# Kernel optimization log

Hardware: AMD Instinct MI355X
Metric: run time of the kernel (lower is better)

Reference implementation:

```python
import jax, jax.numpy as jnp
import numpy as np

B, T, D, H = 2, 2048, 1024, 16
HD = D // H  # head_dim = 64


def setup_inputs() -> dict:
    key = jax.random.key(0)
    ks = jax.random.split(key, 6)
    x = jax.random.normal(ks[0], (B, T, D), dtype=jnp.float32)
    wq = jax.random.normal(ks[1], (D, D), dtype=jnp.float32) * (D ** -0.5)
    wk = jax.random.normal(ks[2], (D, D), dtype=jnp.float32) * (D ** -0.5)
    wv = jax.random.normal(ks[3], (D, D), dtype=jnp.float32) * (D ** -0.5)
    wo = jax.random.normal(ks[4], (D, D), dtype=jnp.float32) * (D ** -0.5)
    # RoPE tables: standard inverse-frequency angles, shape [T, head_dim]
    inv_freq = 1.0 / (10000.0 ** (jnp.arange(0, HD, 2, dtype=jnp.float32) / HD))
    ang = jnp.arange(T, dtype=jnp.float32)[:, None] * inv_freq[None, :]  # [T, HD/2]
    ang = jnp.concatenate([ang, ang], axis=-1)  # [T, HD]
    cos, sin = jnp.cos(ang), jnp.sin(ang)
    # causal mask [1,1,T,T]: True where attention is allowed
    mask = jnp.tril(jnp.ones((T, T), dtype=bool))[None, None]
    return {"x": x, "wq": wq, "wk": wk, "wv": wv, "wo": wo,
            "cos": cos, "sin": sin, "mask": mask}


def rotate_half(u):
    u1, u2 = jnp.split(u, 2, axis=-1)
    return jnp.concatenate([-u2, u1], axis=-1)


def reference(x, wq, wk, wv, wo, cos, sin, mask):
    b, t, c = x.shape
    # projections (nn.Linear: y = x @ W^T), reshape to [B, H, T, HD]
    def proj(w):
        return (x @ w.T).reshape(b, t, H, HD).transpose(0, 2, 1, 3)
    q, k, v = proj(wq), proj(wk), proj(wv)
    # inline RoPE: cos/sin broadcast [1,1,T,HD]
    co = cos[:t][None, None]
    si = sin[:t][None, None]
    q = q * co + rotate_half(q) * si
    k = k * co + rotate_half(k) * si
    # scaled dot-product attention with causal mask
    att = jnp.einsum("bhqd,bhkd->bhqk", q, k) * (HD ** -0.5)
    att = jnp.where(mask[:, :, :t, :t], att, -jnp.inf)
    att = jax.nn.softmax(att, axis=-1)
    out = jnp.einsum("bhqk,bhkd->bhqd", att, v)
    out = out.transpose(0, 2, 1, 3).reshape(b, t, c)
    return out @ wo.T
```

## Files before the change

### kernel.cpp

```cpp
#include <hip/hip_runtime.h>
#include <hip/hip_bf16.h>
#include <type_traits>

#define B_  2
#define T_  2048
#define D_  1024
#define H_  16
#define HD_ 64

typedef __attribute__((ext_vector_type(8))) short bf16x8;
typedef __attribute__((ext_vector_type(4))) float f32x4;

__device__ __forceinline__ unsigned short f2b(float x) {
  union { __hip_bfloat16 h; unsigned short u; } c;
  c.h = __float2bfloat16(x);
  return c.u;
}

__device__ __forceinline__ void ld_g2l_16(const unsigned short* g, unsigned short* l) {
  auto gp = (const __attribute__((address_space(1))) unsigned int*)g;
  auto lp = (__attribute__((address_space(3))) unsigned int*)l;
  __builtin_amdgcn_global_load_lds(gp, lp, 16, 0, 0);
}

__device__ __forceinline__ void cast_job(int blk, const float* __restrict__ x,
                                         const float* __restrict__ wq, const float* __restrict__ wk,
                                         const float* __restrict__ wv, const float* __restrict__ wo,
                                         unsigned short* __restrict__ xb,
                                         unsigned short* __restrict__ wp) {
  const float* src;
  unsigned short* dst;
  size_t off;
  if (blk < 2048) {
    src = x; dst = xb; off = (size_t)blk * 2048;
  } else {
    int t = (blk - 2048) >> 9;
    int r = (blk - 2048) & 511;
    src = (t == 0) ? wq : (t == 1) ? wk : (t == 2) ? wv : wo;
    dst = wp + (size_t)t * 1048576;
    off = (size_t)r * 2048;
  }
  size_t i = off + threadIdx.x * 8;
  float4 a = *(const float4*)(src + i);
  float4 b = *(const float4*)(src + i + 4);
  unsigned short h[8] = {f2b(a.x), f2b(a.y), f2b(a.z), f2b(a.w),
                         f2b(b.x), f2b(b.y), f2b(b.z), f2b(b.w)};
  *(uint4*)(dst + i) = *(uint4*)h;
}

template <typename OutT, int MROWS>
__device__ __forceinline__ void gemm_core(unsigned short* __restrict__ shm,
                                          const unsigned short* __restrict__ A,
                                          const unsigned short* __restrict__ Bw,
                                          OutT* __restrict__ C, int K, int Ldc,
                                          int rope_mode, const float* __restrict__ cosT,
                                          const float* __restrict__ sinT, int tok0) {
  constexpr int MT = MROWS / 32;
  constexpr int ASZ = MROWS * 32;
  const int tid = threadIdx.x;
  const int lane = tid & 63;
  const int w = tid >> 6;
  const int m16 = lane & 15;
  const int quad = lane >> 4;
  const int wm = w >> 1, wn = w & 1;
  const int rl = lane >> 2;
  const int cl = (lane & 3) * 8;

  f32x4 acc[MT][4];
#pragma unroll
  for (int i = 0; i < MT; i++)
#pragma unroll
    for (int j = 0; j < 4; j++) acc[i][j] = (f32x4){0.f, 0.f, 0.f, 0.f};

  auto stage = [&](int it, int bs) {
    int k0 = it * 32;
#pragma unroll
    for (int t = 0; t < MROWS / 64; t++) {
      int seg = w * 16 + t * 64;
      ld_g2l_16(A + (size_t)(seg + rl) * K + k0 + cl, shm + bs * ASZ + seg * 32);
    }
#pragma unroll
    for (int j2 = 0; j2 < 2; j2++) {
      int seg = w * 32 + j2 * 16;
      ld_g2l_16(Bw + (size_t)(seg + rl) * K + k0 + cl, shm + 2 * ASZ + bs * 4096 + seg * 32);
    }
  };

  const int nit = K / 32;
  stage(0, 0);
  __syncthreads();
  for (int it = 0; it < nit; it++) {
    int cur = it & 1;
    if (it + 1 < nit) stage(it + 1, cur ^ 1);
    bf16x8 af[MT], bfr[4];
#pragma unroll
    for (int mt = 0; mt < MT; mt++)
      af[mt] = *(const bf16x8*)(shm + cur * ASZ + (wm * (MT * 16) + mt * 16 + m16) * 32 + quad * 8);
#pragma unroll
    for (int nt = 0; nt < 4; nt++)
      bfr[nt] = *(const bf16x8*)(shm + 2 * ASZ + cur * 4096 + (wn * 64 + nt * 16 + m16) * 32 + quad * 8);
#pragma unroll
    for (int mt = 0; mt < MT; mt++)
#pragma unroll
      for (int nt = 0; nt < 4; nt++)
        acc[mt][nt] = __builtin_amdgcn_mfma_f32_16x16x32_bf16(af[mt], bfr[nt], acc[mt][nt], 0, 0, 0);
    __syncthreads();
  }

  if (rope_mode == 3) {
    if constexpr (std::is_same_v<OutT, unsigned short> && MROWS == 64) {
#pragma unroll
      for (int mt = 0; mt < MT; mt++)
#pragma unroll
        for (int nt = 0; nt < 4; nt++) {
          int lc = wn * 64 + nt * 16 + m16;
          int s  = wm * 8 + mt * 4 + quad;
          int ph = s ^ (lc & 15);
          unsigned short pk[4] = {f2b(acc[mt][nt][0]), f2b(acc[mt][nt][1]),
                                  f2b(acc[mt][nt][2]), f2b(acc[mt][nt][3])};
          *(uint2*)&shm[lc * 64 + ph * 4] = *(uint2*)pk;
        }
      __syncthreads();
#pragma unroll
      for (int i = 0; i < 8; i++) {
        int li = i * 256 + tid;
        int r = li >> 4, c2 = li & 15;
        int ph = c2 ^ (r & 15);
        *(uint2*)(C + (size_t)r * T_ + c2 * 4) = *(const uint2*)&shm[r * 64 + ph * 4];
      }
    }
    return;
  }

  if (rope_mode == 1 || rope_mode == 2) {
    float scale = (rope_mode == 2) ? 0.18033688011112042f : 1.f;
#pragma unroll
    for (int mt = 0; mt < MT; mt++)
#pragma unroll
      for (int reg = 0; reg < 4; reg++) {
        int t = (tok0 + wm * (MT * 16) + mt * 16 + quad * 4 + reg) & (T_ - 1);
#pragma unroll
        for (int nt = 0; nt < 2; nt++) {
          int d = nt * 16 + m16;
          float co = cosT[t * HD_ + d] * scale;
          float si = sinT[t * HD_ + d] * scale;
          float lo = acc[mt][nt][reg], hi = acc[mt][nt + 2][reg];
          acc[mt][nt][reg]     = lo * co - hi * si;
          acc[mt][nt + 2][reg] = hi * co + lo * si;
        }
      }
  }
#pragma unroll
  for (int mt = 0; mt < MT; mt++)
#pragma unroll
    for (int nt = 0; nt < 4; nt++)
#pragma unroll
      for (int reg = 0; reg < 4; reg++) {
        OutT* p = C + (size_t)(wm * (MT * 16) + mt * 16 + quad * 4 + reg) * Ldc + wn * 64 + nt * 16 + m16;
        if constexpr (std::is_same_v<OutT, float>) *p = acc[mt][nt][reg];
        else *p = f2b(acc[mt][nt][reg]);
      }
}

__device__ __forceinline__ void qkv_job(unsigned short* shm, int nb, int bm,
                                        const unsigned short* __restrict__ xb,
                                        const unsigned short* __restrict__ wp,
                                        unsigned short* __restrict__ qkv,
                                        const float* __restrict__ cosT,
                                        const float* __restrict__ sinT) {
  const int mi = nb >> 3;
  const int bn = (nb & 7) * 128;
  if (mi == 2) {
    unsigned short* Cv = qkv + 2 * (4096ull * D_) +
                         (size_t)(bm >> 11) * (size_t)(H_ * HD_) * T_ +
                         (size_t)bn * T_ + (bm & (T_ - 1));
    gemm_core<unsigned short, 64>(shm, xb + (size_t)bm * D_,
                                  wp + (size_t)(2 * 1024 + bn) * D_,
                                  Cv, D_, T_, 3, nullptr, nullptr, bm);
  } else {
    const int rope_mode = (mi == 0) ? 2 : 1;
    gemm_core<unsigned short, 64>(shm, xb + (size_t)bm * D_,
                                  wp + (size_t)(mi * 1024 + bn) * D_,
                                  qkv + (size_t)mi * (4096ull * D_) + (size_t)bm * D_ + bn,
                                  D_, D_, rope_mode, cosT, sinT, bm);
  }
}

__device__ __forceinline__ void attn_job(unsigned short* pool, int x,
                                         const unsigned short* __restrict__ Q,
                                         const unsigned short* __restrict__ K,
                                         const unsigned short* __restrict__ VT,
                                         unsigned short* __restrict__ O) {
  unsigned short* qp = pool;
  unsigned short* ks = pool + 4096;
  unsigned short* vs = pool + 4096 + 8192;

  const int tid = threadIdx.x;
  const int lane = tid & 63;
  const int w = tid >> 6;
  const int m16 = lane & 15;
  const int quad = lane >> 4;
  const int swz = m16 & 7;
  const int pc0 = quad ^ swz;
  const int pc1 = pc0 ^ 4;

  const int qt = 31 - (x >> 5);
  const int bh = x & 31;
  const int b = bh >> 4, h = bh & 15;
  const int q0 = qt * 64;

  const unsigned short* Qb = Q + ((size_t)b * T_ + q0) * D_ + h * HD_;
  const unsigned short* Kb = K + (size_t)b * T_ * D_ + h * HD_;
  const unsigned short* VTb = VT + ((size_t)b * H_ + h) * HD_ * T_;

#pragma unroll
  for (int i = 0; i < 2; i++) {
    int idx = tid + i * 256;
    int r = idx >> 3, c = idx & 7;
    *(bf16x8*)&qp[r * 64 + ((c ^ (r & 7)) * 8)] = *(const bf16x8*)(Qb + (size_t)r * D_ + c * 8);
  }

  auto stage_kv = [&](int kt, int bs) {
    int rs = lane >> 3;
    int cs = ((lane & 7) ^ rs) * 8;
    int gr = w * 16 + rs;
    ld_g2l_16(Kb + (size_t)(kt * 64 + gr) * D_ + cs,      ks + bs * 4096 + (w * 16) * 64);
    ld_g2l_16(Kb + (size_t)(kt * 64 + gr + 8) * D_ + cs,  ks + bs * 4096 + (w * 16 + 8) * 64);
    ld_g2l_16(VTb + (size_t)gr * T_ + kt * 64 + cs,       vs + bs * 4096 + (w * 16) * 64);
    ld_g2l_16(VTb + (size_t)(gr + 8) * T_ + kt * 64 + cs, vs + bs * 4096 + (w * 16 + 8) * 64);
  };

  f32x4 o_acc[4];
#pragma unroll
  for (int dt = 0; dt < 4; dt++) o_acc[dt] = (f32x4){0.f, 0.f, 0.f, 0.f};
  float m_i = -1e30f, l_i = 0.f;
  const int row = w * 16 + m16;
  const int rs7 = row & 7;
  const int rg = q0 + row;

  const short one_bf = (short)0x3F80;
  bf16x8 ones = {one_bf, one_bf, one_bf, one_bf, one_bf, one_bf, one_bf, one_bf};

  stage_kv(0, 0);
  __syncthreads();
  bf16x8 q_frag[2];
  q_frag[0] = *(const bf16x8*)&qp[row * 64 + ((quad ^ rs7) * 8)];
  q_frag[1] = *(const bf16x8*)&qp[row * 64 + (((4 + quad) ^ rs7) * 8)];

  for (int t = 0; t <= qt; t++) {
    int cur = t & 1;
    if (t < qt) stage_kv(t + 1, cur ^ 1);

    const unsigned short* kc = ks + cur * 4096;
    const unsigned short* vc = vs + cur * 4096;
    f32x4 sf[4];
    __builtin_amdgcn_s_setprio(1);
#pragma unroll
    for (int jt = 0; jt < 4; jt++) {
      bf16x8 a0 = *(const bf16x8*)&kc[(jt * 16 + m16) * 64 + pc0 * 8];
      bf16x8 a1 = *(const bf16x8*)&kc[(jt * 16 + m16) * 64 + pc1 * 8];
      f32x4 acc = (f32x4){0.f, 0.f, 0.f, 0.f};
      acc = __builtin_amdgcn_mfma_f32_16x16x32_bf16(a0, q_frag[0], acc, 0, 0, 0);
      acc = __builtin_amdgcn_mfma_f32_16x16x32_bf16(a1, q_frag[1], acc, 0, 0, 0);
      sf[jt] = acc;
    }
    __builtin_amdgcn_s_setprio(0);
    if (t == qt) {
#pragma unroll
      for (int jt = 0; jt < 4; jt++)
#pragma unroll
        for (int reg = 0; reg < 4; reg++) {
          int jg = t * 64 + jt * 16 + quad * 4 + reg;
          if (jg > rg) sf[jt][reg] = -1e30f;
        }
    }
    float mx = sf[0][0];
#pragma unroll
    for (int jt = 0; jt < 4; jt++)
#pragma unroll
      for (int reg = 0; reg < 4; reg++) mx = fmaxf(mx, sf[jt][reg]);
    mx = fmaxf(mx, __shfl_xor(mx, 16, 64));
    mx = fmaxf(mx, __shfl_xor(mx, 32, 64));
    if (!__all(mx <= m_i + 8.f)) {
      float mn = fmaxf(m_i, mx);
      float alpha = exp2f(m_i - mn);
      l_i *= alpha;
#pragma unroll
      for (int dt = 0; dt < 4; dt++)
#pragma unroll
        for (int reg = 0; reg < 4; reg++) o_acc[dt][reg] *= alpha;
      m_i = mn;
    }
    float p[4][4];
#pragma unroll
    for (int jt = 0; jt < 4; jt++)
#pragma unroll
      for (int reg = 0; reg < 4; reg++)
        p[jt][reg] = exp2f(sf[jt][reg] - m_i);
#pragma unroll
    for (int jt = 0; jt < 4; jt++) {
      unsigned short pk[4] = {f2b(p[jt][0]), f2b(p[jt][1]), f2b(p[jt][2]), f2b(p[jt][3])};
      int cL = jt * 2 + (quad >> 1);
      *(uint2*)&qp[row * 64 + ((cL ^ rs7) * 8) + (quad & 1) * 4] = *(uint2*)pk;
    }
    bf16x8 bp0 = *(const bf16x8*)&qp[row * 64 + ((quad ^ rs7) * 8)];
    bf16x8 bp1 = *(const bf16x8*)&qp[row * 64 + (((4 + quad) ^ rs7) * 8)];
    f32x4 lacc = (f32x4){0.f, 0.f, 0.f, 0.f};
    lacc = __builtin_amdgcn_mfma_f32_16x16x32_bf16(ones, bp0, lacc, 0, 0, 0);
    lacc = __builtin_amdgcn_mfma_f32_16x16x32_bf16(ones, bp1, lacc, 0, 0, 0);
    __builtin_amdgcn_s_setprio(1);
#pragma unroll
    for (int dt = 0; dt < 4; dt++) {
      int rowd = dt * 16 + m16;
      bf16x8 a0 = *(const bf16x8*)&vc[rowd * 64 + pc0 * 8];
      bf16x8 a1 = *(const bf16x8*)&vc[rowd * 64 + pc1 * 8];
      o_acc[dt] = __builtin_amdgcn_mfma_f32_16x16x32_bf16(a0, bp0, o_acc[dt], 0, 0, 0);
      o_acc[dt] = __builtin_amdgcn_mfma_f32_16x16x32_bf16(a1, bp1, o_acc[dt], 0, 0, 0);
    }
    __builtin_amdgcn_s_setprio(0);
    l_i += lacc[0];
    __syncthreads();
  }

  float inv = 1.f / l_i;
#pragma unroll
  for (int dt = 0; dt < 4; dt++) {
    unsigned short ok[4];
#pragma unroll
    for (int reg = 0; reg < 4; reg++) ok[reg] = f2b(o_acc[dt][reg] * inv);
    int cL = dt * 2 + (quad >> 1);
    *(uint2*)&qp[row * 64 + ((cL ^ rs7) * 8) + (quad & 1) * 4] = *(uint2*)ok;
  }
  __syncthreads();
  unsigned short* Ob = O + ((size_t)b * T_ + q0) * D_ + h * HD_;
#pragma unroll
  for (int i = 0; i < 2; i++) {
    int idx = tid + i * 256;
    int r = idx >> 3, c = idx & 7;
    *(bf16x8*)(Ob + (size_t)r * D_ + c * 8) = *(const bf16x8*)&qp[r * 64 + ((c ^ (r & 7)) * 8)];
  }
}

__global__ void __launch_bounds__(256)
cast_all(const float* __restrict__ x, const float* __restrict__ wq,
         const float* __restrict__ wk, const float* __restrict__ wv,
         const float* __restrict__ wo, unsigned short* __restrict__ xb,
         unsigned short* __restrict__ wp) {
  cast_job(blockIdx.x, x, wq, wk, wv, wo, xb, wp);
}

__global__ void __launch_bounds__(256, 6)
gemm_qkv(const unsigned short* __restrict__ xb, const unsigned short* __restrict__ wp,
         unsigned short* __restrict__ qkv, const float* __restrict__ cosT,
         const float* __restrict__ sinT) {
  __shared__ __align__(16) unsigned short shm[12288];
  qkv_job(shm, blockIdx.x, blockIdx.y * 64, xb, wp, qkv, cosT, sinT);
}

__global__ void __launch_bounds__(256)
gemm_out(const unsigned short* __restrict__ Ab, const unsigned short* __restrict__ wob,
         float* __restrict__ C) {
  __shared__ __align__(16) unsigned short shm[12288];
  const int bn = blockIdx.x * 128;
  const int bm = blockIdx.y * 64;
  gemm_core<float, 64>(shm, Ab + (size_t)bm * D_, wob + (size_t)bn * D_,
                       C + (size_t)bm * D_ + bn, D_, D_, 0, nullptr, nullptr, 0);
}

__global__ void __launch_bounds__(256, 4)
attn_kernel(const unsigned short* __restrict__ Q, const unsigned short* __restrict__ K,
            const unsigned short* __restrict__ VT, unsigned short* __restrict__ O) {
  __shared__ __align__(16) unsigned short pool[20480];
  attn_job(pool, blockIdx.x, Q, K, VT, O);
}

extern "C" void kernel_launch(void* const* d_in, const int* in_sizes, int n_in,
                              void* d_out, int out_size, void* d_ws, size_t ws_size,
                              hipStream_t stream) {
  const float* x    = (const float*)d_in[0];
  const float* wq   = (const float*)d_in[1];
  const float* wk   = (const float*)d_in[2];
  const float* wv   = (const float*)d_in[3];
  const float* wo   = (const float*)d_in[4];
  const float* cosT = (const float*)d_in[5];
  const float* sinT = (const float*)d_in[6];
  float* out = (float*)d_out;

  const size_t NTOK = (size_t)B_ * T_;
  const size_t SZ   = NTOK * D_;
  unsigned short* xb   = (unsigned short*)d_ws;
  unsigned short* Wp   = xb + SZ;
  unsigned short* QKVh = Wp + 4 * 1048576;
  unsigned short* Ab   = QKVh + 3 * SZ;

  cast_all<<<4096, 256, 0, stream>>>(x, wq, wk, wv, wo, xb, Wp);
  gemm_qkv<<<dim3(24, 64), 256, 0, stream>>>(xb, Wp, QKVh, cosT, sinT);
  attn_kernel<<<1024, 256, 0, stream>>>(QKVh, QKVh + SZ, QKVh + 2 * SZ, Ab);
  gemm_out<<<dim3(8, 64), 256, 0, stream>>>(Ab, Wp + 3 * 1048576, out);
}
```

Baseline: 204.5 us.

## Double GEMM K-tile to 64 with XOR-swizzled LDS layout

The shared GEMM core now stages 64-wide K slices instead of 32, halving the number of main-loop iterations and barriers, and issues two MFMAs per fragment pair per iteration. The LDS layout switches to 64-element rows with an XOR swizzle on 16-byte chunks, meant to avoid bank conflicts on the fragment reads. The QKV and output GEMM kernels double their shared buffers to fit the larger tiles, and their occupancy hint drops to 3 blocks, which lowers the number of resident waves available to hide latency.

```diff
diff --git a/kernel.cpp b/kernel.cpp
--- a/kernel.cpp
+++ b/kernel.cpp
@@ -56,15 +56,19 @@
                                           int rope_mode, const float* __restrict__ cosT,
                                           const float* __restrict__ sinT, int tok0) {
   constexpr int MT = MROWS / 32;
-  constexpr int ASZ = MROWS * 32;
+  constexpr int ASZ = MROWS * 64;
+  constexpr int BSZ = 128 * 64;
   const int tid = threadIdx.x;
   const int lane = tid & 63;
   const int w = tid >> 6;
   const int m16 = lane & 15;
   const int quad = lane >> 4;
   const int wm = w >> 1, wn = w & 1;
-  const int rl = lane >> 2;
-  const int cl = (lane & 3) * 8;
+  const int rs = lane >> 3;
+  const int cs8 = ((lane & 7) ^ rs) * 8;
+  const int swz = m16 & 7;
+  const int pc0 = quad ^ swz;
+  const int pc1 = pc0 ^ 4;
 
   f32x4 acc[MT][4];
 #pragma unroll
@@ -73,37 +77,46 @@
     for (int j = 0; j < 4; j++) acc[i][j] = (f32x4){0.f, 0.f, 0.f, 0.f};
 
   auto stage = [&](int it, int bs) {
-    int k0 = it * 32;
-#pragma unroll
-    for (int t = 0; t < MROWS / 64; t++) {
-      int seg = w * 16 + t * 64;
-      ld_g2l_16(A + (size_t)(seg + rl) * K + k0 + cl, shm + bs * ASZ + seg * 32);
-    }
-#pragma unroll
-    for (int j2 = 0; j2 < 2; j2++) {
-      int seg = w * 32 + j2 * 16;
-      ld_g2l_16(Bw + (size_t)(seg + rl) * K + k0 + cl, shm + 2 * ASZ + bs * 4096 + seg * 32);
+    int k0 = it * 64;
+#pragma unroll
+    for (int t = 0; t < MROWS / 32; t++) {
+      int r0 = w * (MROWS / 4) + t * 8;
+      ld_g2l_16(A + (size_t)(r0 + rs) * K + k0 + cs8, shm + bs * ASZ + r0 * 64);
+    }
+#pragma unroll
+    for (int j = 0; j < 4; j++) {
+      int r0 = w * 32 + j * 8;
+      ld_g2l_16(Bw + (size_t)(r0 + rs) * K + k0 + cs8,
+                shm + 2 * ASZ + bs * BSZ + r0 * 64);
     }
   };
 
-  const int nit = K / 32;
+  const int nit = K / 64;
   stage(0, 0);
   __syncthreads();
   for (int it = 0; it < nit; it++) {
     int cur = it & 1;
     if (it + 1 < nit) stage(it + 1, cur ^ 1);
-    bf16x8 af[MT], bfr[4];
+    bf16x8 af[MT][2], bfr[4][2];
+#pragma unroll
+    for (int mt = 0; mt < MT; mt++) {
+      const unsigned short* ab = shm + cur * ASZ + (wm * (MT * 16) + mt * 16 + m16) * 64;
+      af[mt][0] = *(const bf16x8*)(ab + pc0 * 8);
+      af[mt][1] = *(const bf16x8*)(ab + pc1 * 8);
+    }
+#pragma unroll
+    for (int nt = 0; nt < 4; nt++) {
+      const unsigned short* bb = shm + 2 * ASZ + cur * BSZ + (wn * 64 + nt * 16 + m16) * 64;
+      bfr[nt][0] = *(const bf16x8*)(bb + pc0 * 8);
+      bfr[nt][1] = *(const bf16x8*)(bb + pc1 * 8);
+    }
 #pragma unroll
     for (int mt = 0; mt < MT; mt++)
-      af[mt] = *(const bf16x8*)(shm + cur * ASZ + (wm * (MT * 16) + mt * 16 + m16) * 32 + quad * 8);
-#pragma unroll
-    for (int nt = 0; nt < 4; nt++)
-      bfr[nt] = *(const bf16x8*)(shm + 2 * ASZ + cur * 4096 + (wn * 64 + nt * 16 + m16) * 32 + quad * 8);
-#pragma unroll
-    for (int mt = 0; mt < MT; mt++)
-#pragma unroll
-      for (int nt = 0; nt < 4; nt++)
-        acc[mt][nt] = __builtin_amdgcn_mfma_f32_16x16x32_bf16(af[mt], bfr[nt], acc[mt][nt], 0, 0, 0);
+#pragma unroll
+      for (int nt = 0; nt < 4; nt++) {
+        acc[mt][nt] = __builtin_amdgcn_mfma_f32_16x16x32_bf16(af[mt][0], bfr[nt][0], acc[mt][nt], 0, 0, 0);
+        acc[mt][nt] = __builtin_amdgcn_mfma_f32_16x16x32_bf16(af[mt][1], bfr[nt][1], acc[mt][nt], 0, 0, 0);
+      }
     __syncthreads();
   }
 
@@ -221,9 +234,9 @@
   }
 
   auto stage_kv = [&](int kt, int bs) {
-    int rs = lane >> 3;
-    int cs = ((lane & 7) ^ rs) * 8;
-    int gr = w * 16 + rs;
+    int rsv = lane >> 3;
+    int cs = ((lane & 7) ^ rsv) * 8;
+    int gr = w * 16 + rsv;
     ld_g2l_16(Kb + (size_t)(kt * 64 + gr) * D_ + cs,      ks + bs * 4096 + (w * 16) * 64);
     ld_g2l_16(Kb + (size_t)(kt * 64 + gr + 8) * D_ + cs,  ks + bs * 4096 + (w * 16 + 8) * 64);
     ld_g2l_16(VTb + (size_t)gr * T_ + kt * 64 + cs,       vs + bs * 4096 + (w * 16) * 64);
@@ -349,18 +362,18 @@
   cast_job(blockIdx.x, x, wq, wk, wv, wo, xb, wp);
 }
 
-__global__ void __launch_bounds__(256, 6)
+__global__ void __launch_bounds__(256, 3)
 gemm_qkv(const unsigned short* __restrict__ xb, const unsigned short* __restrict__ wp,
          unsigned short* __restrict__ qkv, const float* __restrict__ cosT,
          const float* __restrict__ sinT) {
-  __shared__ __align__(16) unsigned short shm[12288];
+  __shared__ __align__(16) unsigned short shm[24576];
   qkv_job(shm, blockIdx.x, blockIdx.y * 64, xb, wp, qkv, cosT, sinT);
 }
 
-__global__ void __launch_bounds__(256)
+__global__ void __launch_bounds__(256, 3)
 gemm_out(const unsigned short* __restrict__ Ab, const unsigned short* __restrict__ wob,
          float* __restrict__ C) {
-  __shared__ __align__(16) unsigned short shm[12288];
+  __shared__ __align__(16) unsigned short shm[24576];
   const int bn = blockIdx.x * 128;
   const int bm = blockIdx.y * 64;
   gemm_core<float, 64>(shm, Ab + (size_t)bm * D_, wob + (size_t)bn * D_,
```

Result: faster. 188.6 us (-7.8%).
